# Kernel tuning notes

Hardware: AMD Instinct MI355X
Metric: run time of the kernel (lower is better)

## Reference

```python
import jax, jax.numpy as jnp
import numpy as np

B, C, H, W = 32, 512, 64, 64
P = 8            # partition (window) size
HEAD_DIM = 32
N_HEADS = C // HEAD_DIM  # 16
MLP_RATIO = 4
LN_EPS = 1e-5


def _rel_pos_index(p):
    # Swin/MaxViT-style relative position index for a p x p window -> [p*p, p*p]
    coords = np.stack(np.meshgrid(np.arange(p), np.arange(p), indexing='ij'), 0).reshape(2, -1)
    rel = coords[:, :, None] - coords[:, None, :]          # [2, pp, pp]
    rel = rel.transpose(1, 2, 0) + (p - 1)                 # shift to >= 0
    idx = rel[..., 0] * (2 * p - 1) + rel[..., 1]          # [pp, pp]
    return jnp.asarray(idx, jnp.int32)


def setup_inputs() -> dict:
    key = jax.random.key(0)
    ks = jax.random.split(key, 10)
    s = 0.02
    d_ff = MLP_RATIO * C
    inp = {
        'x': jax.random.normal(ks[0], (B, C, H, W), jnp.float32),
        'gamma1': jnp.ones((C,), jnp.float32),
        'beta1': jnp.zeros((C,), jnp.float32),
        'gamma2': jnp.ones((C,), jnp.float32),
        'beta2': jnp.zeros((C,), jnp.float32),
        'qkv_w': jax.random.normal(ks[1], (C, 3 * C), jnp.float32) * s,
        'qkv_b': jnp.zeros((3 * C,), jnp.float32),
        'merge_w': jax.random.normal(ks[2], (C, C), jnp.float32) * s,
        'merge_b': jnp.zeros((C,), jnp.float32),
        'bias_table': jax.random.normal(ks[3], ((2 * P - 1) ** 2, N_HEADS), jnp.float32) * s,
        'w1': jax.random.normal(ks[4], (C, d_ff), jnp.float32) * s,
        'b1': jnp.zeros((d_ff,), jnp.float32),
        'w2': jax.random.normal(ks[5], (d_ff, C), jnp.float32) * s,
        'b2': jnp.zeros((C,), jnp.float32),
        'rel_idx': _rel_pos_index(P),
    }
    return inp


def _layernorm(t, g, b):
    mu = jnp.mean(t, axis=-1, keepdims=True)
    var = jnp.mean(jnp.square(t - mu), axis=-1, keepdims=True)
    return (t - mu) * jax.lax.rsqrt(var + LN_EPS) * g + b


def reference(x, gamma1, beta1, gamma2, beta2, qkv_w, qkv_b, merge_w, merge_b,
              bias_table, w1, b1, w2, b2, rel_idx):
    p, hd, nh = P, HEAD_DIM, N_HEADS
    Bx, Cx, Hx, Wx = x.shape
    hp, wp = Hx // p, Wx // p
    G, PP = hp * wp, p * p

    # --- window partition: [B,C,H,W] -> [B, G, p*p, C] (partition_type='window', no swap)
    xw = x.reshape(Bx, Cx, hp, p, wp, p).transpose(0, 2, 4, 3, 5, 1).reshape(Bx, G, PP, Cx)

    # --- relative-position multi-head attention on norm1(x)
    h = _layernorm(xw, gamma1, beta1)
    qkv = h @ qkv_w + qkv_b                                   # [B,G,PP,3C]
    q, k, v = jnp.split(qkv, 3, axis=-1)
    q = q.reshape(Bx, G, PP, nh, hd) * (hd ** -0.5)
    k = k.reshape(Bx, G, PP, nh, hd)
    v = v.reshape(Bx, G, PP, nh, hd)
    attn = jnp.einsum('bgqhd,bgkhd->bghqk', q, k)             # [B,G,nh,PP,PP]
    bias = bias_table[rel_idx]                                # [PP,PP,nh]
    attn = attn + bias.transpose(2, 0, 1)[None, None]
    attn = jax.nn.softmax(attn, axis=-1)
    o = jnp.einsum('bghqk,bgkhd->bgqhd', attn, v).reshape(Bx, G, PP, Cx)
    xw = xw + (o @ merge_w + merge_b)                          # residual (dropout/SD p=0)

    # --- MLP block on norm2(x)
    h2 = _layernorm(xw, gamma2, beta2)
    m = jax.nn.gelu(h2 @ w1 + b1) @ w2 + b2
    xw = xw + m

    # --- window departition: [B,G,p*p,C] -> [B,C,H,W]
    out = xw.reshape(Bx, hp, wp, p, p, Cx).transpose(0, 5, 1, 3, 2, 4).reshape(Bx, Cx, Hx, Wx)
    return out
```

## Files before the change

kernel.cpp:

```cpp
#include <hip/hip_runtime.h>
#include <stdint.h>

typedef __attribute__((ext_vector_type(8))) short short8;
typedef __attribute__((ext_vector_type(4))) float f32x4;
typedef __attribute__((address_space(3))) void lds_void;
typedef __attribute__((address_space(1))) void gv_void;

static __device__ __forceinline__ float bf2f(unsigned short u) {
    union { uint32_t i; float f; } v; v.i = ((uint32_t)u) << 16; return v.f;
}
static __device__ __forceinline__ unsigned short f2bf(float f) {
    union { float f; uint32_t i; } v; v.f = f;
    uint32_t i = v.i;
    uint32_t r = (i + 0x7fffu + ((i >> 16) & 1u)) >> 16;
    return (unsigned short)r;
}
static __device__ __forceinline__ float fexp(float x) {
    float r;
    asm("v_exp_f32 %0, %1" : "=v"(r) : "v"(x * 1.44269504088896f));
    return r;
}
static __device__ __forceinline__ float frcp(float x) {
    float r;
    asm("v_rcp_f32 %0, %1" : "=v"(r) : "v"(x));
    return r;
}
static __device__ __forceinline__ uint32_t cvtpk(float lo, float hi) {
    uint32_t r;
    asm("v_cvt_pk_bf16_f32 %0, %1, %2" : "=v"(r) : "v"(lo), "v"(hi));
    return r;
}

__global__ void k_detect(const void* __restrict__ g1, int* __restrict__ flag) {
    if (threadIdx.x == 0 && blockIdx.x == 0) {
        const unsigned short* u = (const unsigned short*)g1;
        flag[0] = (u[0] == 0x3F80u) ? 0 : 1;
    }
}

__global__ __launch_bounds__(256) void k_cvt(const void* __restrict__ src,
                                             unsigned short* __restrict__ dst,
                                             int n, const int* __restrict__ flag) {
    int i = blockIdx.x * 256 + threadIdx.x;
    if (i < n) {
        dst[i] = flag[0] ? f2bf(((const float*)src)[i])
                         : ((const unsigned short*)src)[i];
    }
}

__global__ __launch_bounds__(256) void k_transpose(const void* __restrict__ in,
                                                   unsigned short* __restrict__ out,
                                                   int R, int C, const int* __restrict__ flag) {
    __shared__ unsigned short tile[32][33];
    int isf = flag[0];
    int tx = threadIdx.x, ty = threadIdx.y;
    int x = blockIdx.x * 32 + tx;
    int y0 = blockIdx.y * 32;
    for (int j = ty; j < 32; j += 8) {
        size_t idx = (size_t)(y0 + j) * C + x;
        tile[j][tx] = isf ? f2bf(((const float*)in)[idx]) : ((const unsigned short*)in)[idx];
    }
    __syncthreads();
    int x2 = y0 + tx;
    int y20 = blockIdx.x * 32;
    for (int j = ty; j < 32; j += 8)
        out[(size_t)(y20 + j) * R + x2] = tile[tx][j];
}

__global__ __launch_bounds__(256) void k_prep_bias(const void* __restrict__ bias_table,
                                                   const int* __restrict__ rel_idx,
                                                   float* __restrict__ biasb,
                                                   const int* __restrict__ flag) {
    int i = blockIdx.x * 256 + threadIdx.x;
    int isf = flag[0];
    int r  = i & 3, rl = (i >> 2) & 15, qg = (i >> 6) & 3;
    int km = (i >> 8) & 3, qn = (i >> 10) & 3, h = (i >> 12) & 15;
    int q = 16 * qn + rl, k = 16 * km + 4 * qg + r;
    size_t idx = (size_t)rel_idx[q * 64 + k] * 16 + h;
    float v = isf ? ((const float*)bias_table)[idx] : bf2f(((const unsigned short*)bias_table)[idx]);
    biasb[i] = v;
}

__global__ __launch_bounds__(256) void k_partition_ln(const void* __restrict__ x,
                                                      const unsigned short* __restrict__ g1,
                                                      const unsigned short* __restrict__ b1,
                                                      unsigned short* __restrict__ xw,
                                                      unsigned short* __restrict__ h,
                                                      int b0, const int* __restrict__ flag) {
    __shared__ unsigned short tile[64][512];
    int isf = flag[0];
    int bh = blockIdx.x, bl = bh >> 6, hh = bh & 63;
    int b = b0 + bl;
    int tid = threadIdx.x;
    size_t xoff = (((size_t)b * 512) * 64 + hh) * 64;
    int c0 = tid >> 3, ch = tid & 7;
    if (isf) {
        const float* xb = (const float*)x + xoff;
        for (int k = 0; k < 16; ++k) {
            int c = c0 + k * 32;
            f32x4 v0 = *reinterpret_cast<const f32x4*>(xb + (size_t)c * 4096 + ch * 8);
            f32x4 v1 = *reinterpret_cast<const f32x4*>(xb + (size_t)c * 4096 + ch * 8 + 4);
#pragma unroll
            for (int j = 0; j < 4; ++j) tile[ch * 8 + j][c] = f2bf(v0[j]);
#pragma unroll
            for (int j = 0; j < 4; ++j) tile[ch * 8 + 4 + j][c] = f2bf(v1[j]);
        }
    } else {
        const unsigned short* xb = (const unsigned short*)x + xoff;
        for (int k = 0; k < 16; ++k) {
            int c = c0 + k * 32;
            short8 v = *reinterpret_cast<const short8*>(xb + (size_t)c * 4096 + ch * 8);
#pragma unroll
            for (int j = 0; j < 8; ++j) tile[ch * 8 + j][c] = (unsigned short)v[j];
        }
    }
    __syncthreads();
    int w = tid >> 2, q = tid & 3;
    float s = 0.f, s2 = 0.f;
#pragma unroll 4
    for (int j = 0; j < 128; ++j) {
        int c = q * 128 + ((j + 8 * w) & 127);
        float f = bf2f(tile[w][c]);
        s += f; s2 += f * f;
    }
    s += __shfl_xor(s, 1);  s += __shfl_xor(s, 2);
    s2 += __shfl_xor(s2, 1); s2 += __shfl_xor(s2, 2);
    float mu = s * (1.f / 512.f);
    float rstd = rsqrtf(s2 * (1.f / 512.f) - mu * mu + 1e-5f);
    int t = (bl * 64 + (hh >> 3) * 8 + (w >> 3)) * 64 + (hh & 7) * 8 + (w & 7);
    unsigned short* xr = xw + (size_t)t * 512;
    unsigned short* hr = h + (size_t)t * 512;
    for (int cc = q * 128; cc < q * 128 + 128; cc += 8) {
        short8 raw, hn;
#pragma unroll
        for (int j = 0; j < 8; ++j) {
            unsigned short u = tile[w][cc + j];
            raw[j] = (short)u;
            float f = (bf2f(u) - mu) * rstd * bf2f(g1[cc + j]) + bf2f(b1[cc + j]);
            hn[j] = (short)f2bf(f);
        }
        *reinterpret_cast<short8*>(xr + cc) = raw;
        *reinterpret_cast<short8*>(hr + cc) = hn;
    }
}

__global__ __launch_bounds__(256) void k_ln(const unsigned short* __restrict__ in,
                                            const unsigned short* __restrict__ g,
                                            const unsigned short* __restrict__ b,
                                            unsigned short* __restrict__ out) {
    int wid = threadIdx.x >> 6, lane = threadIdx.x & 63;
    size_t t = (size_t)blockIdx.x * 4 + wid;
    short8 v = *reinterpret_cast<const short8*>(in + t * 512 + lane * 8);
    float f[8], s = 0.f, s2 = 0.f;
#pragma unroll
    for (int j = 0; j < 8; ++j) { f[j] = bf2f((unsigned short)v[j]); s += f[j]; s2 += f[j] * f[j]; }
    for (int m = 1; m < 64; m <<= 1) { s += __shfl_xor(s, m); s2 += __shfl_xor(s2, m); }
    float mu = s * (1.f / 512.f);
    float rstd = rsqrtf(s2 * (1.f / 512.f) - mu * mu + 1e-5f);
    short8 ov;
#pragma unroll
    for (int j = 0; j < 8; ++j)
        ov[j] = (short)f2bf((f[j] - mu) * rstd * bf2f(g[lane * 8 + j]) + bf2f(b[lane * 8 + j]));
    *reinterpret_cast<short8*>(out + t * 512 + lane * 8) = ov;
}

template <int MODE>
__global__ __launch_bounds__(512, 1) void k_gemm6(const unsigned short* __restrict__ A,
                                                  const unsigned short* __restrict__ BT,
                                                  const unsigned short* __restrict__ bias,
                                                  const unsigned short* __restrict__ res,
                                                  unsigned short* __restrict__ out,
                                                  unsigned short* __restrict__ vt,
                                                  void* __restrict__ outx,
                                                  int b0, const int* __restrict__ flag,
                                                  int M, int N, int K) {
    __shared__ unsigned short S[65536];
    const int tid = threadIdx.x, lane = tid & 63, wid = tid >> 6;

    int nwg = gridDim.x * gridDim.y;
    int lin = blockIdx.y * gridDim.x + blockIdx.x;
    int swz = (lin & 7) * (nwg >> 3) + (lin >> 3);
    int mt = swz % gridDim.x, nt = swz / gridDim.x;

    const int wr = wid >> 2, wc = wid & 3;
    const int rl = lane & 15, qg = lane >> 4;

    const int strow = tid >> 2;
    const int scb   = (tid & 3) ^ ((tid >> 3) & 3);
    const unsigned short* Agb = A  + ((size_t)mt * 256 + strow) * K + scb * 8;
    const unsigned short* Bgb = BT + ((size_t)nt * 256 + strow) * K + scb * 8;
    const int ldst = strow * 32 + (tid & 3) * 8;

    f32x4 acc[8][4];
#pragma unroll
    for (int mf = 0; mf < 8; ++mf)
#pragma unroll
        for (int nf = 0; nf < 4; ++nf) {
            acc[mf][nf][0] = 0.f; acc[mf][nf][1] = 0.f; acc[mf][nf][2] = 0.f; acc[mf][nf][3] = 0.f;
        }

    const int NH = K >> 5;

    auto stage = [&](int h) {
        int base = (h & 3) * 16384;
#pragma unroll
        for (int s = 0; s < 2; ++s) {
            __builtin_amdgcn_global_load_lds((const gv_void*)(Agb + (size_t)s * 128 * K + h * 32),
                                             (lds_void*)(&S[base + s * 4096 + ldst]), 16, 0, 0);
            __builtin_amdgcn_global_load_lds((const gv_void*)(Bgb + (size_t)s * 128 * K + h * 32),
                                             (lds_void*)(&S[base + 8192 + s * 4096 + ldst]), 16, 0, 0);
        }
    };

    stage(0); stage(1); stage(2);

    const int arow0 = wr * 128 + rl;
    const int brow0 = wc * 64 + rl;
    const int kbr = (qg ^ ((rl >> 1) & 3)) * 8;

    for (int h = 0; h < NH; ++h) {
        const unsigned short* sA = &S[(h & 3) * 16384];
        const unsigned short* sB = sA + 8192;
        if (h + 3 < NH) {
            stage(h + 3);
            asm volatile("s_waitcnt vmcnt(12)" ::: "memory");
        } else if (h + 2 < NH) {
            asm volatile("s_waitcnt vmcnt(8)" ::: "memory");
        } else if (h + 1 < NH) {
            asm volatile("s_waitcnt vmcnt(4)" ::: "memory");
        } else {
            asm volatile("s_waitcnt vmcnt(0)" ::: "memory");
        }
        __builtin_amdgcn_s_barrier();
        asm volatile("" ::: "memory");

        short8 af[8], bfr[4];
#pragma unroll
        for (int nf = 0; nf < 4; ++nf)
            bfr[nf] = *reinterpret_cast<const short8*>(&sB[(brow0 + nf * 16) * 32 + kbr]);
#pragma unroll
        for (int mf = 0; mf < 8; ++mf)
            af[mf] = *reinterpret_cast<const short8*>(&sA[(arow0 + mf * 16) * 32 + kbr]);

        __builtin_amdgcn_s_setprio(1);
#pragma unroll
        for (int mf = 0; mf < 8; ++mf)
#pragma unroll
            for (int nf = 0; nf < 4; ++nf)
                acc[mf][nf] = __builtin_amdgcn_mfma_f32_16x16x32_bf16(af[mf], bfr[nf], acc[mf][nf], 0, 0, 0);
        __builtin_amdgcn_s_setprio(0);

        __builtin_amdgcn_s_barrier();
        asm volatile("" ::: "memory");
    }

    const int PST = 264;
    unsigned short* pb = (unsigned short*)S;
    float bz[4];
#pragma unroll
    for (int nf = 0; nf < 4; ++nf) bz[nf] = bf2f(bias[nt * 256 + wc * 64 + nf * 16 + rl]);
    int row_l = tid >> 4, cbl = (tid & 15) * 16;
    int growb = mt * 256 + (row_l >> 4) * 128 + (row_l & 15);
    size_t gcol = (size_t)nt * 256 + cbl;
    const int isf = (MODE == 3) ? flag[0] : 0;

#pragma unroll
    for (int mf = 0; mf < 8; ++mf) {
        __syncthreads();
#pragma unroll
        for (int nf = 0; nf < 4; ++nf)
#pragma unroll
            for (int r = 0; r < 4; ++r) {
                float v = acc[mf][nf][r] + bz[nf];
                if (MODE == 2) {
                    float z = 0.7978845608f * (v + 0.044715f * v * v * v);
                    float e = fexp(-2.0f * z);
                    v = v * frcp(1.f + e);
                }
                if (MODE == 3) {
                    size_t rowg = (size_t)(mt * 256 + wr * 128 + mf * 16 + qg * 4 + r);
                    v += bf2f(res[rowg * N + nt * 256 + wc * 64 + nf * 16 + rl]);
                }
                pb[(wr * 16 + qg * 4 + r) * PST + wc * 64 + nf * 16 + rl] = f2bf(v);
            }
        __syncthreads();

        if (MODE == 0 && nt >= 4) {
#pragma unroll
            for (int s = 0; s < 2; ++s) {
                int run = tid + 512 * s;
                int c = run & 255, hp = run >> 8, half = hp >> 1, ph = hp & 1;
                int prow = half * 16 + ph * 8;
                short8 v8;
#pragma unroll
                for (int i = 0; i < 8; ++i) v8[i] = (short)pb[(prow + i) * PST + c];
                int t0 = mt * 256 + half * 128 + mf * 16 + ph * 8;
                int cc = nt * 256 + c - 1024;
                int win = t0 >> 6, k0 = t0 & 63;
                *reinterpret_cast<short8*>(&vt[((size_t)(win * 16 + (cc >> 5)) * 32 + (cc & 31)) * 64 + k0]) = v8;
            }
        } else if (MODE == 3) {
#pragma unroll
            for (int s = 0; s < 2; ++s) {
                int run = tid + 512 * s;
                int c = run & 255, hp = run >> 8, half = hp >> 1, ph = hp & 1;
                int prow = half * 16 + ph * 8;
                int t0 = mt * 256 + half * 128 + mf * 16 + ph * 8;
                int ch = nt * 256 + c;
                int b = b0 + (t0 >> 12), win = (t0 >> 6) & 63, py = (t0 >> 3) & 7;
                size_t xoff = ((size_t)(b * 512 + ch)) * 4096 + ((win >> 3) * 8 + py) * 64 + (win & 7) * 8;
                if (isf) {
                    f32x4 a, d;
#pragma unroll
                    for (int i = 0; i < 4; ++i) a[i] = bf2f(pb[(prow + i) * PST + c]);
#pragma unroll
                    for (int i = 0; i < 4; ++i) d[i] = bf2f(pb[(prow + 4 + i) * PST + c]);
                    *reinterpret_cast<f32x4*>((float*)outx + xoff) = a;
                    *reinterpret_cast<f32x4*>((float*)outx + xoff + 4) = d;
                } else {
                    short8 v8;
#pragma unroll
                    for (int i = 0; i < 8; ++i) v8[i] = (short)pb[(prow + i) * PST + c];
                    *reinterpret_cast<short8*>((unsigned short*)outx + xoff) = v8;
                }
            }
        } else {
            size_t go = (size_t)(growb + mf * 16) * N + gcol;
            short8 o1 = *reinterpret_cast<const short8*>(&pb[row_l * PST + cbl]);
            short8 o2 = *reinterpret_cast<const short8*>(&pb[row_l * PST + cbl + 8]);
            if (MODE == 1) {
                short8 r1 = *reinterpret_cast<const short8*>(&res[go]);
                short8 r2 = *reinterpret_cast<const short8*>(&res[go + 8]);
#pragma unroll
                for (int j = 0; j < 8; ++j) {
                    o1[j] = (short)f2bf(bf2f((unsigned short)o1[j]) + bf2f((unsigned short)r1[j]));
                    o2[j] = (short)f2bf(bf2f((unsigned short)o2[j]) + bf2f((unsigned short)r2[j]));
                }
            }
            *reinterpret_cast<short8*>(&out[go]) = o1;
            *reinterpret_cast<short8*>(&out[go + 8]) = o2;
        }
    }
}

__global__ __launch_bounds__(64) void k_attn2(const unsigned short* __restrict__ qkv,
                                              const unsigned short* __restrict__ vt,
                                              const float* __restrict__ biasb,
                                              unsigned short* __restrict__ o) {
    __shared__ unsigned short Pl[64 * 72];
    int blk = blockIdx.x;
    int head = blk & 15, win = blk >> 4;
    size_t T0 = (size_t)win * 64;
    int lane = threadIdx.x;
    int rl = lane & 15, qg = lane >> 4;
    const unsigned short* base = qkv + T0 * 1536;
    int qoff = head * 32, koff = 512 + head * 32;

    short8 kf[4], qf[4];
#pragma unroll
    for (int m = 0; m < 4; ++m) {
        kf[m] = *reinterpret_cast<const short8*>(base + (size_t)(16 * m + rl) * 1536 + koff + qg * 8);
        qf[m] = *reinterpret_cast<const short8*>(base + (size_t)(16 * m + rl) * 1536 + qoff + qg * 8);
    }
    f32x4 st[4][4];
#pragma unroll
    for (int km = 0; km < 4; ++km)
#pragma unroll
        for (int qn = 0; qn < 4; ++qn) { st[km][qn][0] = 0.f; st[km][qn][1] = 0.f; st[km][qn][2] = 0.f; st[km][qn][3] = 0.f; }
#pragma unroll
    for (int km = 0; km < 4; ++km)
#pragma unroll
        for (int qn = 0; qn < 4; ++qn)
            st[km][qn] = __builtin_amdgcn_mfma_f32_16x16x32_bf16(kf[km], qf[qn], st[km][qn], 0, 0, 0);

    const float scale = 0.17677669529663687f;
    const float* bh = biasb + head * 4096 + qg * 64 + rl * 4;
#pragma unroll
    for (int qn = 0; qn < 4; ++qn) {
        float vv[4][4];
        float mx = -3.0e38f;
#pragma unroll
        for (int km = 0; km < 4; ++km) {
            f32x4 b4 = *reinterpret_cast<const f32x4*>(bh + qn * 1024 + km * 256);
#pragma unroll
            for (int r = 0; r < 4; ++r) {
                vv[km][r] = st[km][qn][r] * scale + b4[r];
                mx = fmaxf(mx, vv[km][r]);
            }
        }
        mx = fmaxf(mx, __shfl_xor(mx, 16));
        mx = fmaxf(mx, __shfl_xor(mx, 32));
        float sm = 0.f;
#pragma unroll
        for (int km = 0; km < 4; ++km)
#pragma unroll
            for (int r = 0; r < 4; ++r) { vv[km][r] = fexp(vv[km][r] - mx); sm += vv[km][r]; }
        sm += __shfl_xor(sm, 16);
        sm += __shfl_xor(sm, 32);
        float inv = frcp(sm);
        int q = 16 * qn + rl;
#pragma unroll
        for (int km = 0; km < 4; ++km) {
            uint32_t w0 = cvtpk(vv[km][0] * inv, vv[km][1] * inv);
            uint32_t w1 = cvtpk(vv[km][2] * inv, vv[km][3] * inv);
            uint32_t* p = reinterpret_cast<uint32_t*>(&Pl[q * 72 + 16 * km + 4 * qg]);
            p[0] = w0; p[1] = w1;
        }
    }

    short8 vf[2][2];
    const unsigned short* vb = vt + (size_t)(win * 16 + head) * 2048;
#pragma unroll
    for (int kb = 0; kb < 2; ++kb)
#pragma unroll
        for (int dn = 0; dn < 2; ++dn)
            vf[kb][dn] = *reinterpret_cast<const short8*>(vb + (16 * dn + rl) * 64 + 32 * kb + 8 * qg);

    __syncthreads();

    f32x4 acc[4][2];
#pragma unroll
    for (int qm = 0; qm < 4; ++qm)
#pragma unroll
        for (int dn = 0; dn < 2; ++dn) { acc[qm][dn][0] = 0.f; acc[qm][dn][1] = 0.f; acc[qm][dn][2] = 0.f; acc[qm][dn][3] = 0.f; }

#pragma unroll
    for (int qm = 0; qm < 4; ++qm) {
        short8 a0 = *reinterpret_cast<const short8*>(&Pl[(16 * qm + rl) * 72 + 8 * qg]);
        short8 a1 = *reinterpret_cast<const short8*>(&Pl[(16 * qm + rl) * 72 + 32 + 8 * qg]);
#pragma unroll
        for (int dn = 0; dn < 2; ++dn) {
            acc[qm][dn] = __builtin_amdgcn_mfma_f32_16x16x32_bf16(a0, vf[0][dn], acc[qm][dn], 0, 0, 0);
            acc[qm][dn] = __builtin_amdgcn_mfma_f32_16x16x32_bf16(a1, vf[1][dn], acc[qm][dn], 0, 0, 0);
        }
    }
#pragma unroll
    for (int qm = 0; qm < 4; ++qm)
#pragma unroll
        for (int dn = 0; dn < 2; ++dn)
#pragma unroll
            for (int r = 0; r < 4; ++r)
                o[(T0 + 16 * qm + 4 * qg + r) * 512 + head * 32 + 16 * dn + rl] = f2bf(acc[qm][dn][r]);
}

extern "C" void kernel_launch(void* const* d_in, const int* in_sizes, int n_in,
                              void* d_out, int out_size, void* d_ws, size_t ws_size,
                              hipStream_t stream) {
    const void* x          = d_in[0];
    const void* g1         = d_in[1];
    const void* be1        = d_in[2];
    const void* g2         = d_in[3];
    const void* be2        = d_in[4];
    const void* qkv_w      = d_in[5];
    const void* qkv_b      = d_in[6];
    const void* merge_w    = d_in[7];
    const void* merge_b    = d_in[8];
    const void* bias_table = d_in[9];
    const void* w1         = d_in[10];
    const void* b1         = d_in[11];
    const void* w2         = d_in[12];
    const void* b2         = d_in[13];
    const int*  rel_idx    = (const int*)d_in[14];

    const size_t extra = 8u << 20;
    int CB = 4;
    if (ws_size >= (size_t)32768 * 11264 + extra) CB = 8;
    int nch = 32 / CB;
    size_t tok = (size_t)CB * 4096;

    unsigned short* xw_c     = (unsigned short*)d_ws;
    unsigned short* h_c      = xw_c + tok * 512;
    unsigned short* o_c      = h_c + tok * 512;
    unsigned short* qkv_c    = o_c + tok * 512;
    unsigned short* mid_c    = qkv_c + tok * 1536;
    unsigned short* vt_c     = mid_c + tok * 2048;
    unsigned short* qkv_wT   = vt_c + tok * 512;
    unsigned short* merge_wT = qkv_wT + 1536 * 512;
    unsigned short* w1T      = merge_wT + 512 * 512;
    unsigned short* w2T      = w1T + 2048 * 512;
    unsigned short* vecs     = w2T + 512 * 2048;
    float*          biasb    = (float*)(vecs + 6656);
    int*            flag     = (int*)(biasb + 65536);

    unsigned short* ng1 = vecs + 0,    *nbe1 = vecs + 512;
    unsigned short* ng2 = vecs + 1024, *nbe2 = vecs + 1536;
    unsigned short* nqb = vecs + 2048, *nmb  = vecs + 3584;
    unsigned short* nb1 = vecs + 4096, *nb2  = vecs + 6144;

    k_detect<<<1, 64, 0, stream>>>(g1, flag);
    k_cvt<<<2, 256, 0, stream>>>(g1, ng1, 512, flag);
    k_cvt<<<2, 256, 0, stream>>>(be1, nbe1, 512, flag);
    k_cvt<<<2, 256, 0, stream>>>(g2, ng2, 512, flag);
    k_cvt<<<2, 256, 0, stream>>>(be2, nbe2, 512, flag);
    k_cvt<<<6, 256, 0, stream>>>(qkv_b, nqb, 1536, flag);
    k_cvt<<<2, 256, 0, stream>>>(merge_b, nmb, 512, flag);
    k_cvt<<<8, 256, 0, stream>>>(b1, nb1, 2048, flag);
    k_cvt<<<2, 256, 0, stream>>>(b2, nb2, 512, flag);
    k_transpose<<<dim3(48, 16), dim3(32, 8), 0, stream>>>(qkv_w, qkv_wT, 512, 1536, flag);
    k_transpose<<<dim3(16, 16), dim3(32, 8), 0, stream>>>(merge_w, merge_wT, 512, 512, flag);
    k_transpose<<<dim3(64, 16), dim3(32, 8), 0, stream>>>(w1, w1T, 512, 2048, flag);
    k_transpose<<<dim3(16, 64), dim3(32, 8), 0, stream>>>(w2, w2T, 2048, 512, flag);
    k_prep_bias<<<256, 256, 0, stream>>>(bias_table, rel_idx, biasb, flag);

    int mtiles = (int)(tok / 256);
    int M = (int)tok;
    for (int c = 0; c < nch; ++c) {
        int b0 = c * CB;
        k_partition_ln<<<CB * 64, 256, 0, stream>>>(x, ng1, nbe1, xw_c, h_c, b0, flag);
        k_gemm6<0><<<dim3(mtiles, 6), 512, 0, stream>>>(h_c, qkv_wT, nqb, nullptr, qkv_c, vt_c,
                                                        nullptr, 0, flag, M, 1536, 512);
        k_attn2<<<CB * 1024, 64, 0, stream>>>(qkv_c, vt_c, biasb, o_c);
        k_gemm6<1><<<dim3(mtiles, 2), 512, 0, stream>>>(o_c, merge_wT, nmb, xw_c, xw_c, nullptr,
                                                        nullptr, 0, flag, M, 512, 512);
        k_ln<<<(int)(tok / 4), 256, 0, stream>>>(xw_c, ng2, nbe2, h_c);
        k_gemm6<2><<<dim3(mtiles, 8), 512, 0, stream>>>(h_c, w1T, nb1, nullptr, mid_c, nullptr,
                                                        nullptr, 0, flag, M, 2048, 512);
        k_gemm6<3><<<dim3(mtiles, 2), 512, 0, stream>>>(mid_c, w2T, nb2, xw_c, qkv_c, nullptr,
                                                        d_out, b0, flag, M, 512, 2048);
    }
}
```

Measured before the change: 1.964 ms.

## Double-buffer GEMM register fragments and split departition into separate kernel

The GEMM main loop now loads the next K-step's LDS fragments into a second register set while MFMAs run on the current set. This cuts the barrier count per step to one and lets stage prefetch start right after that barrier. The final MLP GEMM's scattered departition epilogue is removed. It now writes token-major output with the residual add, and a new LDS-tiled departition kernel then writes coalesced NCHW output. This trades an extra kernel and a round trip through memory for the intermediate against more coalesced global writes and a simpler GEMM epilogue. Holding two fragment sets raises register pressure.

```diff
diff --git a/kernel.cpp b/kernel.cpp
--- a/kernel.cpp
+++ b/kernel.cpp
@@ -165,14 +165,12 @@
 }
 
 template <int MODE>
-__global__ __launch_bounds__(512, 1) void k_gemm6(const unsigned short* __restrict__ A,
+__global__ __launch_bounds__(512, 1) void k_gemm7(const unsigned short* __restrict__ A,
                                                   const unsigned short* __restrict__ BT,
                                                   const unsigned short* __restrict__ bias,
                                                   const unsigned short* __restrict__ res,
                                                   unsigned short* __restrict__ out,
                                                   unsigned short* __restrict__ vt,
-                                                  void* __restrict__ outx,
-                                                  int b0, const int* __restrict__ flag,
                                                   int M, int N, int K) {
     __shared__ unsigned short S[65536];
     const int tid = threadIdx.x, lane = tid & 63, wid = tid >> 6;
@@ -212,46 +210,49 @@
         }
     };
 
-    stage(0); stage(1); stage(2);
-
     const int arow0 = wr * 128 + rl;
     const int brow0 = wc * 64 + rl;
     const int kbr = (qg ^ ((rl >> 1) & 3)) * 8;
 
-    for (int h = 0; h < NH; ++h) {
+    auto readf = [&](int h, short8 (&af)[8], short8 (&bfr)[4]) {
         const unsigned short* sA = &S[(h & 3) * 16384];
         const unsigned short* sB = sA + 8192;
-        if (h + 3 < NH) {
-            stage(h + 3);
-            asm volatile("s_waitcnt vmcnt(12)" ::: "memory");
-        } else if (h + 2 < NH) {
-            asm volatile("s_waitcnt vmcnt(8)" ::: "memory");
-        } else if (h + 1 < NH) {
-            asm volatile("s_waitcnt vmcnt(4)" ::: "memory");
-        } else {
-            asm volatile("s_waitcnt vmcnt(0)" ::: "memory");
-        }
+#pragma unroll
+        for (int nf = 0; nf < 4; ++nf)
+            bfr[nf] = *reinterpret_cast<const short8*>(&sB[(brow0 + nf * 16) * 32 + kbr]);
+#pragma unroll
+        for (int mf = 0; mf < 8; ++mf)
+            af[mf] = *reinterpret_cast<const short8*>(&sA[(arow0 + mf * 16) * 32 + kbr]);
+    };
+
+    auto body = [&](int h, short8 (&uA)[8], short8 (&uB)[4],
+                    short8 (&rA)[8], short8 (&rB)[4]) {
+        if (h + 2 < NH)      { asm volatile("s_waitcnt vmcnt(4)" ::: "memory"); }
+        else if (h + 1 < NH) { asm volatile("s_waitcnt vmcnt(0)" ::: "memory"); }
         __builtin_amdgcn_s_barrier();
         asm volatile("" ::: "memory");
-
-        short8 af[8], bfr[4];
-#pragma unroll
-        for (int nf = 0; nf < 4; ++nf)
-            bfr[nf] = *reinterpret_cast<const short8*>(&sB[(brow0 + nf * 16) * 32 + kbr]);
+        if (h + 3 < NH) stage(h + 3);
+        if (h + 1 < NH) readf(h + 1, rA, rB);
+        __builtin_amdgcn_s_setprio(1);
 #pragma unroll
         for (int mf = 0; mf < 8; ++mf)
-            af[mf] = *reinterpret_cast<const short8*>(&sA[(arow0 + mf * 16) * 32 + kbr]);
-
-        __builtin_amdgcn_s_setprio(1);
-#pragma unroll
-        for (int mf = 0; mf < 8; ++mf)
 #pragma unroll
             for (int nf = 0; nf < 4; ++nf)
-                acc[mf][nf] = __builtin_amdgcn_mfma_f32_16x16x32_bf16(af[mf], bfr[nf], acc[mf][nf], 0, 0, 0);
+                acc[mf][nf] = __builtin_amdgcn_mfma_f32_16x16x32_bf16(uA[mf], uB[nf], acc[mf][nf], 0, 0, 0);
         __builtin_amdgcn_s_setprio(0);
-
-        __builtin_amdgcn_s_barrier();
-        asm volatile("" ::: "memory");
+    };
+
+    stage(0); stage(1); stage(2);
+    asm volatile("s_waitcnt vmcnt(8)" ::: "memory");
+    __builtin_amdgcn_s_barrier();
+    asm volatile("" ::: "memory");
+
+    short8 afA[8], bfA[4], afB[8], bfB[4];
+    readf(0, afA, bfA);
+
+    for (int hh = 0; hh < NH; hh += 2) {
+        body(hh,     afA, bfA, afB, bfB);
+        body(hh + 1, afB, bfB, afA, bfA);
     }
 
     const int PST = 264;
@@ -262,7 +263,6 @@
     int row_l = tid >> 4, cbl = (tid & 15) * 16;
     int growb = mt * 256 + (row_l >> 4) * 128 + (row_l & 15);
     size_t gcol = (size_t)nt * 256 + cbl;
-    const int isf = (MODE == 3) ? flag[0] : 0;
 
 #pragma unroll
     for (int mf = 0; mf < 8; ++mf) {
@@ -277,13 +277,24 @@
                     float e = fexp(-2.0f * z);
                     v = v * frcp(1.f + e);
                 }
-                if (MODE == 3) {
-                    size_t rowg = (size_t)(mt * 256 + wr * 128 + mf * 16 + qg * 4 + r);
-                    v += bf2f(res[rowg * N + nt * 256 + wc * 64 + nf * 16 + rl]);
-                }
                 pb[(wr * 16 + qg * 4 + r) * PST + wc * 64 + nf * 16 + rl] = f2bf(v);
             }
         __syncthreads();
+
+        size_t go = (size_t)(growb + mf * 16) * N + gcol;
+        short8 o1 = *reinterpret_cast<const short8*>(&pb[row_l * PST + cbl]);
+        short8 o2 = *reinterpret_cast<const short8*>(&pb[row_l * PST + cbl + 8]);
+        if (MODE == 1) {
+            short8 r1 = *reinterpret_cast<const short8*>(&res[go]);
+            short8 r2 = *reinterpret_cast<const short8*>(&res[go + 8]);
+#pragma unroll
+            for (int j = 0; j < 8; ++j) {
+                o1[j] = (short)f2bf(bf2f((unsigned short)o1[j]) + bf2f((unsigned short)r1[j]));
+                o2[j] = (short)f2bf(bf2f((unsigned short)o2[j]) + bf2f((unsigned short)r2[j]));
+            }
+        }
+        *reinterpret_cast<short8*>(&out[go]) = o1;
+        *reinterpret_cast<short8*>(&out[go + 8]) = o2;
 
         if (MODE == 0 && nt >= 4) {
 #pragma unroll
@@ -299,46 +310,6 @@
                 int win = t0 >> 6, k0 = t0 & 63;
                 *reinterpret_cast<short8*>(&vt[((size_t)(win * 16 + (cc >> 5)) * 32 + (cc & 31)) * 64 + k0]) = v8;
             }
-        } else if (MODE == 3) {
-#pragma unroll
-            for (int s = 0; s < 2; ++s) {
-                int run = tid + 512 * s;
-                int c = run & 255, hp = run >> 8, half = hp >> 1, ph = hp & 1;
-                int prow = half * 16 + ph * 8;
-                int t0 = mt * 256 + half * 128 + mf * 16 + ph * 8;
-                int ch = nt * 256 + c;
-                int b = b0 + (t0 >> 12), win = (t0 >> 6) & 63, py = (t0 >> 3) & 7;
-                size_t xoff = ((size_t)(b * 512 + ch)) * 4096 + ((win >> 3) * 8 + py) * 64 + (win & 7) * 8;
-                if (isf) {
-                    f32x4 a, d;
-#pragma unroll
-                    for (int i = 0; i < 4; ++i) a[i] = bf2f(pb[(prow + i) * PST + c]);
-#pragma unroll
-                    for (int i = 0; i < 4; ++i) d[i] = bf2f(pb[(prow + 4 + i) * PST + c]);
-                    *reinterpret_cast<f32x4*>((float*)outx + xoff) = a;
-                    *reinterpret_cast<f32x4*>((float*)outx + xoff + 4) = d;
-                } else {
-                    short8 v8;
-#pragma unroll
-                    for (int i = 0; i < 8; ++i) v8[i] = (short)pb[(prow + i) * PST + c];
-                    *reinterpret_cast<short8*>((unsigned short*)outx + xoff) = v8;
-                }
-            }
-        } else {
-            size_t go = (size_t)(growb + mf * 16) * N + gcol;
-            short8 o1 = *reinterpret_cast<const short8*>(&pb[row_l * PST + cbl]);
-            short8 o2 = *reinterpret_cast<const short8*>(&pb[row_l * PST + cbl + 8]);
-            if (MODE == 1) {
-                short8 r1 = *reinterpret_cast<const short8*>(&res[go]);
-                short8 r2 = *reinterpret_cast<const short8*>(&res[go + 8]);
-#pragma unroll
-                for (int j = 0; j < 8; ++j) {
-                    o1[j] = (short)f2bf(bf2f((unsigned short)o1[j]) + bf2f((unsigned short)r1[j]));
-                    o2[j] = (short)f2bf(bf2f((unsigned short)o2[j]) + bf2f((unsigned short)r2[j]));
-                }
-            }
-            *reinterpret_cast<short8*>(&out[go]) = o1;
-            *reinterpret_cast<short8*>(&out[go + 8]) = o2;
         }
     }
 }
@@ -441,6 +412,50 @@
 #pragma unroll
             for (int r = 0; r < 4; ++r)
                 o[(T0 + 16 * qm + 4 * qg + r) * 512 + head * 32 + 16 * dn + rl] = f2bf(acc[qm][dn][r]);
+}
+
+__global__ __launch_bounds__(256) void k_departition(const unsigned short* __restrict__ tok,
+                                                     void* __restrict__ xo,
+                                                     int b0, const int* __restrict__ flag) {
+    __shared__ unsigned short tile[64][512];
+    int isf = flag[0];
+    int bh = blockIdx.x, bl = bh >> 6, hh = bh & 63;
+    int b = b0 + bl;
+    int tid = threadIdx.x;
+    int Tb = (bl * 64 + (hh >> 3) * 8) * 64 + (hh & 7) * 8;
+    for (int k = 0; k < 16; ++k) {
+        int flat = k * 256 + tid;
+        int w = flat >> 6, ch = flat & 63;
+        int t = Tb + (w >> 3) * 64 + (w & 7);
+        short8 v = *reinterpret_cast<const short8*>(tok + (size_t)t * 512 + ch * 8);
+        *reinterpret_cast<short8*>(&tile[w][ch * 8]) = v;
+    }
+    __syncthreads();
+    size_t xoff = (((size_t)b * 512) * 64 + hh) * 64;
+    if (isf) {
+        float* xb = (float*)xo + xoff;
+        for (int k = 0; k < 16; ++k) {
+            int flat = k * 256 + tid;
+            int c = flat >> 3, wc = flat & 7;
+            f32x4 a, d;
+#pragma unroll
+            for (int j = 0; j < 4; ++j) a[j] = bf2f(tile[wc * 8 + j][c]);
+#pragma unroll
+            for (int j = 0; j < 4; ++j) d[j] = bf2f(tile[wc * 8 + 4 + j][c]);
+            *reinterpret_cast<f32x4*>(xb + (size_t)c * 4096 + wc * 8) = a;
+            *reinterpret_cast<f32x4*>(xb + (size_t)c * 4096 + wc * 8 + 4) = d;
+        }
+    } else {
+        unsigned short* xb = (unsigned short*)xo + xoff;
+        for (int k = 0; k < 16; ++k) {
+            int flat = k * 256 + tid;
+            int c = flat >> 3, wc = flat & 7;
+            short8 v;
+#pragma unroll
+            for (int j = 0; j < 8; ++j) v[j] = (short)tile[wc * 8 + j][c];
+            *reinterpret_cast<short8*>(xb + (size_t)c * 4096 + wc * 8) = v;
+        }
+    }
 }
 
 extern "C" void kernel_launch(void* const* d_in, const int* in_sizes, int n_in,
@@ -507,15 +522,12 @@
     for (int c = 0; c < nch; ++c) {
         int b0 = c * CB;
         k_partition_ln<<<CB * 64, 256, 0, stream>>>(x, ng1, nbe1, xw_c, h_c, b0, flag);
-        k_gemm6<0><<<dim3(mtiles, 6), 512, 0, stream>>>(h_c, qkv_wT, nqb, nullptr, qkv_c, vt_c,
-                                                        nullptr, 0, flag, M, 1536, 512);
+        k_gemm7<0><<<dim3(mtiles, 6), 512, 0, stream>>>(h_c, qkv_wT, nqb, nullptr, qkv_c, vt_c, M, 1536, 512);
         k_attn2<<<CB * 1024, 64, 0, stream>>>(qkv_c, vt_c, biasb, o_c);
-        k_gemm6<1><<<dim3(mtiles, 2), 512, 0, stream>>>(o_c, merge_wT, nmb, xw_c, xw_c, nullptr,
-                                                        nullptr, 0, flag, M, 512, 512);
+        k_gemm7<1><<<dim3(mtiles, 2), 512, 0, stream>>>(o_c, merge_wT, nmb, xw_c, xw_c, nullptr, M, 512, 512);
         k_ln<<<(int)(tok / 4), 256, 0, stream>>>(xw_c, ng2, nbe2, h_c);
-        k_gemm6<2><<<dim3(mtiles, 8), 512, 0, stream>>>(h_c, w1T, nb1, nullptr, mid_c, nullptr,
-                                                        nullptr, 0, flag, M, 2048, 512);
-        k_gemm6<3><<<dim3(mtiles, 2), 512, 0, stream>>>(mid_c, w2T, nb2, xw_c, qkv_c, nullptr,
-                                                        d_out, b0, flag, M, 512, 2048);
-    }
-}
+        k_gemm7<2><<<dim3(mtiles, 8), 512, 0, stream>>>(h_c, w1T, nb1, nullptr, mid_c, nullptr, M, 2048, 512);
+        k_gemm7<1><<<dim3(mtiles, 2), 512, 0, stream>>>(mid_c, w2T, nb2, xw_c, qkv_c, nullptr, M, 512, 2048);
+        k_departition<<<CB * 64, 256, 0, stream>>>(qkv_c, d_out, b0, flag);
+    }
+}
```

New measurement: 1.968 ms. About the same (+0.2%).
